# Kernel optimization log

Measured on AMD Instinct MI355X. Metric: run time of the kernel, lower is better.

The kernel has to match this reference:

```python
import jax, jax.numpy as jnp
import numpy as np

MAX_ITERS = 50
EPS_NORM = 1e-8
EPS_SEP = -1e-6


def setup_inputs() -> dict:
    key = jax.random.key(0)
    k1, k2 = jax.random.split(key)
    pointcloud = jax.random.normal(k1, (200000, 3), dtype=jnp.float32)
    targets = jax.random.normal(k2, (256, 3), dtype=jnp.float32)
    return {"pointcloud": pointcloud, "targets": targets}


def reference(pointcloud, targets):
    # pointcloud: [N, d], targets: [M, d]
    N = pointcloud.shape[0]
    M = targets.shape[0]
    p2 = jnp.sum(pointcloud * pointcloud, axis=1)  # [N]
    t2 = jnp.sum(targets * targets, axis=1)        # [M]

    def step(mask, _):
        # squared euclidean distances [M, N] (argmin identical to cdist argmin)
        d2 = t2[:, None] + p2[None, :] - 2.0 * (targets @ pointcloud.T)
        d2 = jnp.where(mask, d2, jnp.inf)
        closest_idx = jnp.argmin(d2, axis=1)           # [M]
        closest_points = pointcloud[closest_idx]       # [M, d]
        a = closest_points - targets
        a = a / (jnp.linalg.norm(a, axis=1, keepdims=True) + EPS_NORM)
        b = jnp.sum(a * closest_points, axis=1)        # [M]
        dot = a @ pointcloud.T - b[:, None]            # [M, N]
        separated = dot >= EPS_SEP
        mask = mask & ~separated
        return mask, (a, b)

    mask0 = jnp.ones((M, N), dtype=bool)
    _, (a_stack, b_stack) = jax.lax.scan(step, mask0, None, length=MAX_ITERS)
    return a_stack, b_stack  # [MAX_ITERS, M, d], [MAX_ITERS, M]
```

## Files before the change

### kernel.cpp

```cpp
#include <hip/hip_runtime.h>
#include <stdint.h>
#include <math.h>

#pragma clang fp contract(off)

#define BLOCK 1024
#define NW (BLOCK / 64)
#define PT 8
#define PB 4
#define MAX_ITERS 50
#define SOLO_CAP 2048
#define EPS_NORM 1e-8f
#define EPS_SEP (-1e-6f)

__global__ void pack_points(const float* __restrict__ pc,
                            float4* __restrict__ pk, int N) {
    const int i = blockIdx.x * blockDim.x + threadIdx.x;
    if (i < N) {
        const float x = pc[3*i+0], y = pc[3*i+1], z = pc[3*i+2];
        float4 v; v.x = x; v.y = y; v.z = z;
        v.w = x*x + y*y + z*z;
        pk[i] = v;
    }
}

template <bool PACKED>
__global__ __launch_bounds__(BLOCK) void convex_plane_kernel(
    const float* __restrict__ pc, const float4* __restrict__ pk,
    const float* __restrict__ tg,
    float* __restrict__ out, int N, int M, int CAP, int stepsA)
{
    extern __shared__ uint32_t smem[];
    const int tid  = threadIdx.x;
    const int lane = tid & 63;
    const int wv   = tid >> 6;
    const int m    = blockIdx.x;

    const int maskW = stepsA * (PT * BLOCK / 32);
    uint32_t* mask  = smem;
    int*      list  = (int*)(smem + maskW);
    float*    red_d = (float*)(list + CAP);
    int*      red_i = (int*)(red_d + NW);
    int*      cw    = red_i + NW;
    int*      bcast = cw + NW;
    int*      cnt   = bcast + 2;

    const float tx = tg[3*m+0], ty = tg[3*m+1], tz = tg[3*m+2];
    const float t2 = tx*tx + ty*ty + tz*tz;

    float* out_a = out;
    float* out_b = out + (size_t)MAX_ITERS * (size_t)M * 3;

    auto ldp = [&](int ip, float& x, float& y, float& z, float& w) {
        if constexpr (PACKED) {
            const float4 v = pk[ip];
            x = v.x; y = v.y; z = v.z; w = v.w;
        } else {
            const float* p = pc + 3 * (size_t)ip;
            x = p[0]; y = p[1]; z = p[2];
            w = x*x + y*y + z*z;
        }
    };

    auto finish = [&](float dmin, int imin, int mycnt, bool cntFromCursor) -> int2 {
        #pragma unroll
        for (int off = 32; off > 0; off >>= 1) {
            float od = __shfl_down(dmin, off, 64);
            int   oi = __shfl_down(imin, off, 64);
            int   oc = __shfl_down(mycnt, off, 64);
            if (od < dmin || (od == dmin && oi < imin)) { dmin = od; imin = oi; }
            mycnt += oc;
        }
        if (lane == 0) { red_d[wv] = dmin; red_i[wv] = imin; cw[wv] = mycnt; }
        __syncthreads();
        if (wv == 0) {
            float bd = (lane < NW) ? red_d[lane] : INFINITY;
            int   bi = (lane < NW) ? red_i[lane] : 0;
            int   c  = (lane < NW) ? cw[lane]    : 0;
            #pragma unroll
            for (int off = 8; off > 0; off >>= 1) {
                float od = __shfl_down(bd, off, 64);
                int   oi = __shfl_down(bi, off, 64);
                int   oc = __shfl_down(c,  off, 64);
                if (od < bd || (od == bd && oi < bi)) { bd = od; bi = oi; }
                c += oc;
            }
            if (lane == 0) { bcast[0] = bi; bcast[1] = cntFromCursor ? cnt[0] : c; }
        }
        __syncthreads();
        int2 r; r.x = bcast[0]; r.y = bcast[1];
        return r;
    };

    auto scanA = [&](int mode, bool build,
                     float ax, float ay, float az, float b) -> int2 {
        if (tid == 0) cnt[0] = 0;
        __syncthreads();
        float dmin = INFINITY;
        int   imin = 0;
        int   mycnt = 0;
        for (int s = 0; s < stepsA; ++s) {
            const int ib    = s * PT * BLOCK + tid;
            const int wbase = s * (PT * BLOCK / 32);
            uint32_t live = 0;
            if (mode == 2) {
                #pragma unroll
                for (int j = 0; j < PT; ++j) {
                    uint32_t w = mask[wbase + j * (BLOCK / 32) + (tid >> 5)];
                    live |= ((w >> (tid & 31)) & 1u) << j;
                }
            } else {
                #pragma unroll
                for (int j = 0; j < PT; ++j)
                    if (ib + j * BLOCK < N) live |= (1u << j);
            }
            float px[PT], py[PT], pz[PT], pw[PT];
            #pragma unroll
            for (int j = 0; j < PT; ++j) {
                int ip = ib + j * BLOCK;
                ip = ip < N ? ip : N - 1;
                ldp(ip, px[j], py[j], pz[j], pw[j]);
            }
            uint32_t keepm = 0;
            #pragma unroll
            for (int j = 0; j < PT; ++j) {
                if ((live >> j) & 1u) {
                    bool keep;
                    if (mode == 0) keep = true;
                    else {
                        float dt = ax*px[j] + ay*py[j] + az*pz[j] - b;
                        keep = (dt < EPS_SEP);
                    }
                    if (keep) {
                        keepm |= (1u << j);
                        float tp = tx*px[j] + ty*py[j] + tz*pz[j];
                        float d2 = t2 + pw[j] - 2.0f*tp;
                        if (d2 < dmin) { dmin = d2; imin = ib + j * BLOCK; }
                    }
                }
            }
            if (mode != 0) {
                #pragma unroll
                for (int j = 0; j < PT; ++j) {
                    unsigned long long bal = __ballot(((keepm >> j) & 1u) != 0u);
                    const int widx = wbase + j * (BLOCK / 32) + (wv << 1);
                    if (lane == 0)       mask[widx]     = (uint32_t)bal;
                    else if (lane == 32) mask[widx + 1] = (uint32_t)(bal >> 32);
                }
            }
            mycnt += (int)__popc(keepm);
            if (build) {
                int c = (int)__popc(keepm);
                int incl = c;
                #pragma unroll
                for (int off = 1; off < 64; off <<= 1) {
                    int o = __shfl_up(incl, off, 64);
                    if (lane >= off) incl += o;
                }
                const int excl = incl - c;
                const int tot  = __shfl(incl, 63, 64);
                int wb = 0;
                if (lane == 0) wb = atomicAdd(cnt, tot);
                wb = __shfl(wb, 0, 64);
                int pos = wb + excl;
                #pragma unroll
                for (int j = 0; j < PT; ++j) {
                    if ((keepm >> j) & 1u) {
                        if (pos < CAP) list[pos] = ib + j * BLOCK;
                        ++pos;
                    }
                }
            }
        }
        return finish(dmin, imin, mycnt, false);
    };

    auto scanB = [&](int count, float ax, float ay, float az, float b) -> int2 {
        if (tid == 0) cnt[0] = 0;
        __syncthreads();
        float dmin = INFINITY;
        int   imin = 0;
        const int per = BLOCK * PB;
        const int bsteps = (count + per - 1) / per;
        for (int s = 0; s < bsteps; ++s) {
            int jv[PB]; float d2v[PB];
            uint32_t keepm = 0;
            #pragma unroll
            for (int q = 0; q < PB; ++q) {
                const int e = s * per + q * BLOCK + tid;
                if (e < count) {
                    const int j = list[e];
                    jv[q] = j;
                    float px, py, pz, p2;
                    ldp(j, px, py, pz, p2);
                    float dt = ax*px + ay*py + az*pz - b;
                    if (dt < EPS_SEP) {
                        keepm |= (1u << q);
                        float tp = tx*px + ty*py + tz*pz;
                        d2v[q] = t2 + p2 - 2.0f*tp;
                    }
                }
            }
            __syncthreads();
            int c = (int)__popc(keepm);
            int incl = c;
            #pragma unroll
            for (int off = 1; off < 64; off <<= 1) {
                int o = __shfl_up(incl, off, 64);
                if (lane >= off) incl += o;
            }
            const int excl = incl - c;
            const int tot  = __shfl(incl, 63, 64);
            int wb = 0;
            if (lane == 0) wb = atomicAdd(cnt, tot);
            wb = __shfl(wb, 0, 64);
            int pos = wb + excl;
            #pragma unroll
            for (int q = 0; q < PB; ++q) {
                if ((keepm >> q) & 1u) {
                    list[pos] = jv[q];
                    if (d2v[q] < dmin || (d2v[q] == dmin && jv[q] < imin)) {
                        dmin = d2v[q]; imin = jv[q];
                    }
                    ++pos;
                }
            }
        }
        __syncthreads();
        return finish(dmin, imin, 0, true);
    };

    bool comp = false;
    int2 rc = scanA(0, false, 0.f, 0.f, 0.f, 0.f);
    int idx = rc.x, count = rc.y;

    for (int k = 0; k < MAX_ITERS; ++k) {
        if (comp && count <= SOLO_CAP) {
            if (wv != 0) return;
            for (; k < MAX_ITERS; ++k) {
                float cx, cy, cz, cw4;
                ldp(idx, cx, cy, cz, cw4);
                const float vx = cx - tx, vy = cy - ty, vz = cz - tz;
                const float nrm = sqrtf(vx*vx + vy*vy + vz*vz);
                const float den = nrm + EPS_NORM;
                const float ax = vx / den, ay = vy / den, az = vz / den;
                const float b  = ax*cx + ay*cy + az*cz;
                if (count == 0) {
                    for (int q = lane; q < MAX_ITERS - k; q += 64) {
                        const int kk = k + q;
                        const size_t oa = ((size_t)kk * M + m) * 3;
                        out_a[oa+0] = ax; out_a[oa+1] = ay; out_a[oa+2] = az;
                        out_b[(size_t)kk * M + m] = b;
                    }
                    return;
                }
                if (lane == 0) {
                    const size_t oa = ((size_t)k * M + m) * 3;
                    out_a[oa+0] = ax; out_a[oa+1] = ay; out_a[oa+2] = az;
                    out_b[(size_t)k * M + m] = b;
                }
                if (k + 1 < MAX_ITERS) {
                    float dmin = INFINITY; int imin = 0; int wcur = 0;
                    for (int e0 = 0; e0 < count; e0 += 64) {
                        const int e = e0 + lane;
                        bool keep = false; int j = 0; float d2v = 0.f;
                        if (e < count) {
                            j = list[e];
                            float px, py, pz, p2;
                            ldp(j, px, py, pz, p2);
                            float dt = ax*px + ay*py + az*pz - b;
                            if (dt < EPS_SEP) {
                                keep = true;
                                float tp = tx*px + ty*py + tz*pz;
                                d2v = t2 + p2 - 2.0f*tp;
                            }
                        }
                        unsigned long long bal = __ballot(keep);
                        int pos = wcur + (int)__popcll(bal & ((1ull << lane) - 1ull));
                        if (keep) {
                            list[pos] = j;
                            if (d2v < dmin || (d2v == dmin && j < imin)) {
                                dmin = d2v; imin = j;
                            }
                        }
                        wcur += (int)__popcll(bal);
                    }
                    #pragma unroll
                    for (int off = 32; off > 0; off >>= 1) {
                        float od = __shfl_down(dmin, off, 64);
                        int   oi = __shfl_down(imin, off, 64);
                        if (od < dmin || (od == dmin && oi < imin)) { dmin = od; imin = oi; }
                    }
                    idx = __shfl(imin, 0, 64);
                    count = wcur;
                }
            }
            return;
        }

        float cx, cy, cz, cw4;
        ldp(idx, cx, cy, cz, cw4);
        const float vx = cx - tx, vy = cy - ty, vz = cz - tz;
        const float nrm = sqrtf(vx*vx + vy*vy + vz*vz);
        const float den = nrm + EPS_NORM;
        const float ax = vx / den, ay = vy / den, az = vz / den;
        const float b  = ax*cx + ay*cy + az*cz;

        if (count == 0) {
            for (int q = tid; q < MAX_ITERS - k; q += BLOCK) {
                const int kk = k + q;
                const size_t oa = ((size_t)kk * M + m) * 3;
                out_a[oa+0] = ax; out_a[oa+1] = ay; out_a[oa+2] = az;
                out_b[(size_t)kk * M + m] = b;
            }
            return;
        }
        if (tid == 0) {
            const size_t oa = ((size_t)k * M + m) * 3;
            out_a[oa+0] = ax; out_a[oa+1] = ay; out_a[oa+2] = az;
            out_b[(size_t)k * M + m] = b;
        }
        if (k + 1 < MAX_ITERS) {
            if (comp) {
                rc = scanB(count, ax, ay, az, b);
            } else {
                const bool build = (count <= 2 * CAP);
                rc = scanA(k == 0 ? 1 : 2, build, ax, ay, az, b);
                if (build && rc.y <= CAP) comp = true;
            }
            idx = rc.x; count = rc.y;
        }
    }
}

extern "C" void kernel_launch(void* const* d_in, const int* in_sizes, int n_in,
                              void* d_out, int out_size, void* d_ws, size_t ws_size,
                              hipStream_t stream) {
    const float* pc = (const float*)d_in[0];
    const float* tg = (const float*)d_in[1];
    float* out = (float*)d_out;
    const int N = in_sizes[0] / 3;
    const int M = in_sizes[1] / 3;
    const int stepsA = (N + BLOCK * PT - 1) / (BLOCK * PT);
    const size_t maskB  = (size_t)stepsA * (PT * BLOCK / 32) * sizeof(uint32_t);
    const size_t fixedB = NW * (2 * sizeof(int) + sizeof(float)) + 3 * sizeof(int);
    const size_t packB  = (size_t)N * sizeof(float4);
    const bool packed = (d_ws != nullptr) && (ws_size >= packB);

    int CAP = 32768;
    size_t smem = maskB + (size_t)CAP * sizeof(int) + fixedB;
    const void* fn = packed ? (const void*)convex_plane_kernel<true>
                            : (const void*)convex_plane_kernel<false>;
    if (hipFuncSetAttribute(fn, hipFuncAttributeMaxDynamicSharedMemorySize,
                            (int)smem) != hipSuccess) {
        CAP = 8192;
        smem = maskB + (size_t)CAP * sizeof(int) + fixedB;
    }
    if (packed) {
        float4* pk = (float4*)d_ws;
        pack_points<<<(N + 255) / 256, 256, 0, stream>>>(pc, pk, N);
        convex_plane_kernel<true><<<M, BLOCK, smem, stream>>>(
            pc, pk, tg, out, N, M, CAP, stepsA);
    } else {
        convex_plane_kernel<false><<<M, BLOCK, smem, stream>>>(
            pc, nullptr, tg, out, N, M, CAP, stepsA);
    }
}
```

Baseline: 480.8 us.

## Add SoA point layout and per-block staggered scan start

When the workspace is large enough, the packing kernel also writes separate x/y/z arrays and the main kernel loads those instead of float4, recomputing the squared norm in registers. Each block now begins its pass over point tiles at a hashed offset, so blocks do not all read the same region at the same time. Because tiles are visited out of order, the argmin update adds an explicit lowest-index tie-break. The changes trade fewer bytes per load for extra ALU and a larger workspace footprint.

After: 597.6 us. 24.3% more time.

```diff
diff --git a/kernel.cpp b/kernel.cpp
--- a/kernel.cpp
+++ b/kernel.cpp
@@ -14,20 +14,24 @@
 #define EPS_SEP (-1e-6f)
 
 __global__ void pack_points(const float* __restrict__ pc,
-                            float4* __restrict__ pk, int N) {
+                            float4* __restrict__ pk,
+                            float* __restrict__ sx, float* __restrict__ sy,
+                            float* __restrict__ sz, int N, int mode) {
     const int i = blockIdx.x * blockDim.x + threadIdx.x;
     if (i < N) {
         const float x = pc[3*i+0], y = pc[3*i+1], z = pc[3*i+2];
         float4 v; v.x = x; v.y = y; v.z = z;
         v.w = x*x + y*y + z*z;
         pk[i] = v;
+        if (mode >= 2) { sx[i] = x; sy[i] = y; sz[i] = z; }
     }
 }
 
-template <bool PACKED>
+template <int MODE>
 __global__ __launch_bounds__(BLOCK) void convex_plane_kernel(
     const float* __restrict__ pc, const float4* __restrict__ pk,
-    const float* __restrict__ tg,
+    const float* __restrict__ sx, const float* __restrict__ sy,
+    const float* __restrict__ sz, const float* __restrict__ tg,
     float* __restrict__ out, int N, int M, int CAP, int stepsA)
 {
     extern __shared__ uint32_t smem[];
@@ -45,6 +49,8 @@
     int*      bcast = cw + NW;
     int*      cnt   = bcast + 2;
 
+    const int s0 = (int)(((uint32_t)m * 2654435761u) % (uint32_t)stepsA);
+
     const float tx = tg[3*m+0], ty = tg[3*m+1], tz = tg[3*m+2];
     const float t2 = tx*tx + ty*ty + tz*tz;
 
@@ -52,7 +58,7 @@
     float* out_b = out + (size_t)MAX_ITERS * (size_t)M * 3;
 
     auto ldp = [&](int ip, float& x, float& y, float& z, float& w) {
-        if constexpr (PACKED) {
+        if constexpr (MODE >= 1) {
             const float4 v = pk[ip];
             x = v.x; y = v.y; z = v.z; w = v.w;
         } else {
@@ -100,8 +106,9 @@
         int   imin = 0;
         int   mycnt = 0;
         for (int s = 0; s < stepsA; ++s) {
-            const int ib    = s * PT * BLOCK + tid;
-            const int wbase = s * (PT * BLOCK / 32);
+            int sa = s + s0; if (sa >= stepsA) sa -= stepsA;
+            const int ib    = sa * PT * BLOCK + tid;
+            const int wbase = sa * (PT * BLOCK / 32);
             uint32_t live = 0;
             if (mode == 2) {
                 #pragma unroll
@@ -115,11 +122,23 @@
                     if (ib + j * BLOCK < N) live |= (1u << j);
             }
             float px[PT], py[PT], pz[PT], pw[PT];
-            #pragma unroll
-            for (int j = 0; j < PT; ++j) {
-                int ip = ib + j * BLOCK;
-                ip = ip < N ? ip : N - 1;
-                ldp(ip, px[j], py[j], pz[j], pw[j]);
+            if constexpr (MODE == 2) {
+                #pragma unroll
+                for (int j = 0; j < PT; ++j) {
+                    int ip = ib + j * BLOCK;
+                    ip = ip < N ? ip : N - 1;
+                    px[j] = sx[ip]; py[j] = sy[ip]; pz[j] = sz[ip];
+                }
+                #pragma unroll
+                for (int j = 0; j < PT; ++j)
+                    pw[j] = px[j]*px[j] + py[j]*py[j] + pz[j]*pz[j];
+            } else {
+                #pragma unroll
+                for (int j = 0; j < PT; ++j) {
+                    int ip = ib + j * BLOCK;
+                    ip = ip < N ? ip : N - 1;
+                    ldp(ip, px[j], py[j], pz[j], pw[j]);
+                }
             }
             uint32_t keepm = 0;
             #pragma unroll
@@ -135,7 +154,10 @@
                         keepm |= (1u << j);
                         float tp = tx*px[j] + ty*py[j] + tz*pz[j];
                         float d2 = t2 + pw[j] - 2.0f*tp;
-                        if (d2 < dmin) { dmin = d2; imin = ib + j * BLOCK; }
+                        const int i = ib + j * BLOCK;
+                        if (d2 < dmin || (d2 == dmin && i < imin)) {
+                            dmin = d2; imin = i;
+                        }
                     }
                 }
             }
@@ -344,25 +366,40 @@
     const int stepsA = (N + BLOCK * PT - 1) / (BLOCK * PT);
     const size_t maskB  = (size_t)stepsA * (PT * BLOCK / 32) * sizeof(uint32_t);
     const size_t fixedB = NW * (2 * sizeof(int) + sizeof(float)) + 3 * sizeof(int);
-    const size_t packB  = (size_t)N * sizeof(float4);
-    const bool packed = (d_ws != nullptr) && (ws_size >= packB);
+    const size_t need16 = (size_t)N * sizeof(float4);
+    const size_t need28 = need16 + 3 * (size_t)N * sizeof(float);
+
+    int wsmode = 0;
+    if (d_ws && ws_size >= need28) wsmode = 2;
+    else if (d_ws && ws_size >= need16) wsmode = 1;
+
+    float4* pk = (float4*)d_ws;
+    float*  sxp = (float*)((char*)d_ws + need16);
+    float*  syp = sxp + N;
+    float*  szp = syp + N;
 
     int CAP = 32768;
     size_t smem = maskB + (size_t)CAP * sizeof(int) + fixedB;
-    const void* fn = packed ? (const void*)convex_plane_kernel<true>
-                            : (const void*)convex_plane_kernel<false>;
+    const void* fn = (wsmode == 2) ? (const void*)convex_plane_kernel<2>
+                   : (wsmode == 1) ? (const void*)convex_plane_kernel<1>
+                                   : (const void*)convex_plane_kernel<0>;
     if (hipFuncSetAttribute(fn, hipFuncAttributeMaxDynamicSharedMemorySize,
                             (int)smem) != hipSuccess) {
         CAP = 8192;
         smem = maskB + (size_t)CAP * sizeof(int) + fixedB;
     }
-    if (packed) {
-        float4* pk = (float4*)d_ws;
-        pack_points<<<(N + 255) / 256, 256, 0, stream>>>(pc, pk, N);
-        convex_plane_kernel<true><<<M, BLOCK, smem, stream>>>(
-            pc, pk, tg, out, N, M, CAP, stepsA);
+    if (wsmode >= 1) {
+        pack_points<<<(N + 255) / 256, 256, 0, stream>>>(pc, pk, sxp, syp, szp,
+                                                         N, wsmode);
+    }
+    if (wsmode == 2) {
+        convex_plane_kernel<2><<<M, BLOCK, smem, stream>>>(
+            pc, pk, sxp, syp, szp, tg, out, N, M, CAP, stepsA);
+    } else if (wsmode == 1) {
+        convex_plane_kernel<1><<<M, BLOCK, smem, stream>>>(
+            pc, pk, nullptr, nullptr, nullptr, tg, out, N, M, CAP, stepsA);
     } else {
-        convex_plane_kernel<false><<<M, BLOCK, smem, stream>>>(
-            pc, nullptr, tg, out, N, M, CAP, stepsA);
+        convex_plane_kernel<0><<<M, BLOCK, smem, stream>>>(
+            pc, nullptr, nullptr, nullptr, nullptr, tg, out, N, M, CAP, stepsA);
     }
 }
```
